# Kernel tuning notes

Hardware: AMD Instinct MI355X
Metric: run time of the kernel (lower is better)

The kernel has to match this reference:

```python
import jax, jax.numpy as jnp
import numpy as np

B, T, I, H = 32, 512, 512, 512
G = 4 * H
TEMP = 2.0 / 3.0
LIM_A, LIM_B = -0.1, 1.1
EPSILON = 1e-6


def setup_inputs() -> dict:
    key = jax.random.key(0)
    ks = jax.random.split(key, 16)
    mask_mu = float(np.log(1 - 0.2) - np.log(0.2))  # droprate_init = 0.2
    inp = {
        "seq": jax.random.normal(ks[0], (B, T, I), jnp.float32),
        "w_ih": jax.random.normal(ks[1], (G, I), jnp.float32) * (1.0 / np.sqrt(I)),
        "w_hh": jax.random.normal(ks[2], (G, H), jnp.float32) * (1.0 / np.sqrt(H)),
        "b_ih": jnp.zeros((G,), jnp.float32),
        "b_hh": jnp.zeros((G,), jnp.float32),
        "mask_ih": mask_mu + 0.01 * jax.random.normal(ks[3], (G, I), jnp.float32),
        "mask_hh": mask_mu + 0.01 * jax.random.normal(ks[4], (G, H), jnp.float32),
        "mask_bih": mask_mu + 0.01 * jax.random.normal(ks[5], (G,), jnp.float32),
        "mask_bhh": mask_mu + 0.01 * jax.random.normal(ks[6], (G,), jnp.float32),
        "eps_ih": jax.random.uniform(ks[7], (B, G, I), jnp.float32, EPSILON, 1 - EPSILON),
        "eps_hh": jax.random.uniform(ks[8], (B, G, H), jnp.float32, EPSILON, 1 - EPSILON),
        "eps_bih": jax.random.uniform(ks[9], (B, G), jnp.float32, EPSILON, 1 - EPSILON),
        "eps_bhh": jax.random.uniform(ks[10], (B, G), jnp.float32, EPSILON, 1 - EPSILON),
    }
    return inp


def _sample_weight(eps, mask, param):
    # quantile of stretched concrete, then hard-sigmoid gate, applied to param.
    # eps: [B, ...], mask/param: [...] broadcast over batch.
    y = jax.nn.sigmoid((jnp.log(eps) - jnp.log1p(-eps) + mask) / TEMP)
    z = jnp.clip(y * (LIM_B - LIM_A) + LIM_A, 0.0, 1.0)
    return z * param  # [B, ...]


def reference(seq, w_ih, w_hh, b_ih, b_hh,
              mask_ih, mask_hh, mask_bih, mask_bhh,
              eps_ih, eps_hh, eps_bih, eps_bhh):
    # Per-batch-element L0-gated weights (training-mode sampling with fixed eps)
    Wih = _sample_weight(eps_ih, mask_ih, w_ih)      # [B, 4H, I]
    Whh = _sample_weight(eps_hh, mask_hh, w_hh)      # [B, 4H, H]
    Bih = _sample_weight(eps_bih, mask_bih, b_ih)    # [B, 4H]
    Bhh = _sample_weight(eps_bhh, mask_bhh, b_hh)    # [B, 4H]
    bias = Bih + Bhh                                  # [B, 4H]

    h0 = jnp.zeros((seq.shape[0], H), seq.dtype)
    c0 = jnp.zeros((seq.shape[0], H), seq.dtype)

    # Precompute input projections for all timesteps: [T, B, 4H]
    x_proj = jnp.einsum('bti,bgi->tbg', seq, Wih) + bias[None]

    def step(carry, xp_t):
        h, c = carry
        gates = xp_t + jnp.einsum('bh,bgh->bg', h, Whh)  # [B, 4H]
        i, f, g, o = jnp.split(gates, 4, axis=-1)        # torch order: i,f,g,o
        i = jax.nn.sigmoid(i)
        f = jax.nn.sigmoid(f)
        g = jnp.tanh(g)
        o = jax.nn.sigmoid(o)
        c = f * c + i * g
        h = o * jnp.tanh(c)
        return (h, c), h

    (h_n, c_n), hs = jax.lax.scan(step, (h0, c0), x_proj)
    output = jnp.transpose(hs, (1, 0, 2))  # [B, T, H]
    # torch code cats per-sample hiddens [1,1,H] along dim 0 -> [B, 1, H]
    return output, h_n[:, None, :], c_n[:, None, :]
```

## Files before the change

### kernel.cpp

```cpp
#include <hip/hip_runtime.h>

#define NB 32
#define NT 512
#define NI 512
#define NH 512
#define NG 2048
#define GH (NG*NH)
#define BTH ((size_t)NB*NT*NH)
#define BH  (NB*NH)

typedef unsigned int uint;
typedef unsigned long long u64;
typedef _Float16 v2h __attribute__((ext_vector_type(2)));

#define OFF_XPROJ 0
#define SZ_XPROJ  ((size_t)NB*NT*NG*2)
#define OFF_BIAS  (OFF_XPROJ + SZ_XPROJ)
#define SZ_BIAS   ((size_t)NB*NG*4)
#define OFF_HP    (OFF_BIAS + SZ_BIAS)
#define SZ_HP     ((size_t)2*NB*256*8)

__device__ __forceinline__ float bf2f(unsigned short u) {
    union { uint i; float f; } v; v.i = ((uint)u) << 16; return v.f;
}
__device__ __forceinline__ unsigned short f2bf(float f) {
    union { uint i; float f; } v; v.f = f;
    uint r = v.i + 0x7FFFu + ((v.i >> 16) & 1u);
    return (unsigned short)(r >> 16);
}
__device__ __forceinline__ uint pkf16(float a, float b) {
    auto p = __builtin_amdgcn_cvt_pkrtz(a, b);
    return __builtin_bit_cast(uint, p);
}
__device__ __forceinline__ float dot2(uint wu, uint hu, float c) {
#if __has_builtin(__builtin_amdgcn_fdot2)
    return __builtin_amdgcn_fdot2(__builtin_bit_cast(v2h, wu),
                                  __builtin_bit_cast(v2h, hu), c, false);
#else
    v2h a = __builtin_bit_cast(v2h, wu), b = __builtin_bit_cast(v2h, hu);
    return c + (float)a[0] * (float)b[0] + (float)a[1] * (float)b[1];
#endif
}
__device__ __forceinline__ float gate_z(float eps, float m) {
    float u = (__logf(eps) - __logf(1.0f - eps) + m) * 1.5f;
    float y = 1.0f / (1.0f + __expf(-u));
    float z = fmaf(y, 1.2f, -0.1f);
    return fminf(fmaxf(z, 0.0f), 1.0f);
}
__device__ __forceinline__ float sigmoidf_(float x) {
    return 1.0f / (1.0f + __expf(-x));
}
__device__ __forceinline__ float tanhf_(float x) {
    return 1.0f - 2.0f / (__expf(2.0f * x) + 1.0f);
}
__device__ __forceinline__ int hswz(int kg, int r, int u) {
    return (kg << 4) + (((r + (kg >> 1)) & 3) << 2) + u;
}

__global__ __launch_bounds__(256) void k_bias(
    const float* __restrict__ eb1, const float* __restrict__ eb2,
    const float* __restrict__ mb1, const float* __restrict__ mb2,
    const float* __restrict__ b1, const float* __restrict__ b2,
    float* __restrict__ bias) {
    int idx = blockIdx.x * 256 + threadIdx.x;
    int g = idx & (NG - 1);
    bias[idx] = gate_z(eb1[idx], mb1[g]) * b1[g] + gate_z(eb2[idx], mb2[g]) * b2[g];
}

__global__ __launch_bounds__(256) void k_xproj(
    const float* __restrict__ seq, const float* __restrict__ eps_ih,
    const float* __restrict__ mask_ih, const float* __restrict__ w_ih,
    const float* __restrict__ bias, unsigned short* __restrict__ xproj) {
    __shared__ float As[128 * 33];
    __shared__ float Ws[32 * 68];
    int g0 = blockIdx.x * 64;
    int t0 = blockIdx.y * 128;
    int b  = blockIdx.z;
    int tid = threadIdx.x;
    int gq = tid & 15;
    int rq = tid >> 4;
    float acc[4][8];
#pragma unroll
    for (int c = 0; c < 4; ++c)
#pragma unroll
        for (int k = 0; k < 8; ++k) acc[c][k] = 0.0f;

    for (int i0 = 0; i0 < NI; i0 += 32) {
        __syncthreads();
#pragma unroll
        for (int k = 0; k < 4; ++k) {
            int e = (tid + (k << 8)) << 2;
            int r = e >> 5, c = e & 31;
            float4 v = *(const float4*)(seq + (b * NT + t0 + r) * NI + i0 + c);
            As[r * 33 + c    ] = v.x;
            As[r * 33 + c + 1] = v.y;
            As[r * 33 + c + 2] = v.z;
            As[r * 33 + c + 3] = v.w;
        }
#pragma unroll
        for (int k = 0; k < 2; ++k) {
            int e = (tid + (k << 8)) << 2;
            int gr = e >> 5, c = e & 31;
            int mo = (g0 + gr) * NI + i0 + c;
            int eo = b * GH + mo;
            float4 ev = *(const float4*)(eps_ih + eo);
            float4 mv = *(const float4*)(mask_ih + mo);
            float4 wv = *(const float4*)(w_ih + mo);
            Ws[(c    ) * 68 + gr] = gate_z(ev.x, mv.x) * wv.x;
            Ws[(c + 1) * 68 + gr] = gate_z(ev.y, mv.y) * wv.y;
            Ws[(c + 2) * 68 + gr] = gate_z(ev.z, mv.z) * wv.z;
            Ws[(c + 3) * 68 + gr] = gate_z(ev.w, mv.w) * wv.w;
        }
        __syncthreads();
#pragma unroll 4
        for (int i = 0; i < 32; ++i) {
            float4 wv = *(const float4*)&Ws[i * 68 + (gq << 2)];
#pragma unroll
            for (int k = 0; k < 8; ++k) {
                float av = As[(rq + (k << 4)) * 33 + i];
                acc[0][k] = fmaf(wv.x, av, acc[0][k]);
                acc[1][k] = fmaf(wv.y, av, acc[1][k]);
                acc[2][k] = fmaf(wv.z, av, acc[2][k]);
                acc[3][k] = fmaf(wv.w, av, acc[3][k]);
            }
        }
    }
    float bs[4];
#pragma unroll
    for (int c = 0; c < 4; ++c) bs[c] = bias[b * NG + g0 + (gq << 2) + c];
#pragma unroll
    for (int k = 0; k < 8; ++k) {
        int r = t0 + rq + (k << 4);
        unsigned short* op = xproj + (b * NT + r) * NG + g0 + (gq << 2);
        union { uint2 v; unsigned short s[4]; } o;
        o.s[0] = f2bf(acc[0][k] + bs[0]);
        o.s[1] = f2bf(acc[1][k] + bs[1]);
        o.s[2] = f2bf(acc[2][k] + bs[2]);
        o.s[3] = f2bf(acc[3][k] + bs[3]);
        *(uint2*)op = o.v;
    }
}

__global__ __launch_bounds__(1024, 4) void k_recur(
    const float* __restrict__ eps, const float* __restrict__ mask,
    const float* __restrict__ w, const unsigned short* __restrict__ xproj,
    u64* __restrict__ hpk, float* __restrict__ out) {
    __shared__ uint hsh[2][256];
    int bb = blockIdx.x;
    int b = bb >> 3, slice = bb & 7;
    int tid = threadIdx.x;
    int wv = tid >> 6, lane = tid & 63;
    int jj = lane >> 4, kg = lane & 15;
    int j = (slice << 6) + (wv << 2) + jj;
    bool leader = (kg == 0);

    uint wreg[4][16];
#pragma unroll
    for (int q = 0; q < 4; ++q) {
        size_t off = (size_t)((q << 9) + j) * NH + (kg << 5);
        const float2* ep = (const float2*)(eps + (size_t)b * GH + off);
        const float2* mp = (const float2*)(mask + off);
        const float2* wp = (const float2*)(w + off);
#pragma unroll
        for (int u = 0; u < 16; ++u) {
            float2 e = ep[u], m = mp[u], ww = wp[u];
            wreg[q][u] = pkf16(gate_z(e.x, m.x) * ww.x,
                               gate_z(e.y, m.y) * ww.y);
        }
    }

    float xp0 = 0.f, xp1 = 0.f, xp2 = 0.f, xp3 = 0.f;
    if (leader) {
        const unsigned short* xq = xproj + ((size_t)(b * NT) << 11) + j;
        xp0 = bf2f(xq[0]); xp1 = bf2f(xq[512]);
        xp2 = bf2f(xq[1024]); xp3 = bf2f(xq[1536]);
    }

    float c = 0.0f;
    for (int t = 0; t < NT; ++t) {
        int par = t & 1;
        if (tid < 256 && !(t > 0 && (tid >> 5) == slice)) {
            const u64* src = hpk + ((size_t)(par * NB + b) << 8) + tid;
            u64 v;
            do {
                v = __hip_atomic_load(src, __ATOMIC_RELAXED, __HIP_MEMORY_SCOPE_AGENT);
            } while ((uint)(v >> 32) != (uint)t);
            hsh[par][hswz(tid >> 4, (tid >> 2) & 3, tid & 3)] = (uint)v;
        }
        __syncthreads();

        float a0 = 0.f, a1 = 0.f, a2 = 0.f, a3 = 0.f;
#pragma unroll
        for (int r = 0; r < 4; ++r) {
            uint4 hv = *(const uint4*)&hsh[par][hswz(kg, r, 0)];
            uint hu[4] = {hv.x, hv.y, hv.z, hv.w};
#pragma unroll
            for (int u = 0; u < 4; ++u) {
                a0 = dot2(wreg[0][(r << 2) + u], hu[u], a0);
                a1 = dot2(wreg[1][(r << 2) + u], hu[u], a1);
                a2 = dot2(wreg[2][(r << 2) + u], hu[u], a2);
                a3 = dot2(wreg[3][(r << 2) + u], hu[u], a3);
            }
        }
#pragma unroll
        for (int off = 8; off > 0; off >>= 1) {
            a0 += __shfl_xor(a0, off);
            a1 += __shfl_xor(a1, off);
            a2 += __shfl_xor(a2, off);
            a3 += __shfl_xor(a3, off);
        }
        if (leader) {
            float gi = a0 + xp0, gf = a1 + xp1, gg = a2 + xp2, go = a3 + xp3;
            c = fmaf(sigmoidf_(gf), c, sigmoidf_(gi) * tanhf_(gg));
            float h = sigmoidf_(go) * tanhf_(c);
            out[((size_t)(b * NT + t) << 9) + j] = h;
            if (t == NT - 1) {
                out[BTH + (size_t)(b << 9) + j] = h;
                out[BTH + BH + (size_t)(b << 9) + j] = c;
            }
            float hpart = __shfl_xor(h, 16);
            if ((lane & 16) == 0) {
                uint pk = pkf16(h, hpart);
                int wd = (slice << 5) + (wv << 1) + (lane >> 5);
                u64 val = ((u64)(uint)(t + 1) << 32) | (u64)pk;
                __hip_atomic_store(hpk + ((size_t)(((t + 1) & 1) * NB + b) << 8) + wd,
                                   val, __ATOMIC_RELAXED, __HIP_MEMORY_SCOPE_AGENT);
                hsh[(t + 1) & 1][hswz(wd >> 4, (wd >> 2) & 3, wd & 3)] = pk;
            }
            if (t + 1 < NT) {
                const unsigned short* xq = xproj + ((size_t)(b * NT + t + 1) << 11) + j;
                xp0 = bf2f(xq[0]); xp1 = bf2f(xq[512]);
                xp2 = bf2f(xq[1024]); xp3 = bf2f(xq[1536]);
            }
        }
    }
}

extern "C" void kernel_launch(void* const* d_in, const int* in_sizes, int n_in,
                              void* d_out, int out_size, void* d_ws, size_t ws_size,
                              hipStream_t stream) {
    const float* seq      = (const float*)d_in[0];
    const float* w_ih     = (const float*)d_in[1];
    const float* w_hh     = (const float*)d_in[2];
    const float* b_ih     = (const float*)d_in[3];
    const float* b_hh     = (const float*)d_in[4];
    const float* mask_ih  = (const float*)d_in[5];
    const float* mask_hh  = (const float*)d_in[6];
    const float* mask_bih = (const float*)d_in[7];
    const float* mask_bhh = (const float*)d_in[8];
    const float* eps_ih   = (const float*)d_in[9];
    const float* eps_hh   = (const float*)d_in[10];
    const float* eps_bih  = (const float*)d_in[11];
    const float* eps_bhh  = (const float*)d_in[12];

    char* ws = (char*)d_ws;
    unsigned short* xproj = (unsigned short*)(ws + OFF_XPROJ);
    float* bias  = (float*)(ws + OFF_BIAS);
    u64*   hpk   = (u64*)(ws + OFF_HP);
    float* out   = (float*)d_out;

    (void)hipMemsetAsync(hpk, 0, (size_t)NB * 256 * 8, stream);

    k_bias<<<dim3(256), dim3(256), 0, stream>>>(eps_bih, eps_bhh, mask_bih, mask_bhh,
                                                b_ih, b_hh, bias);
    k_xproj<<<dim3(NG / 64, NT / 128, NB), dim3(256), 0, stream>>>(
        seq, eps_ih, mask_ih, w_ih, bias, xproj);
    k_recur<<<dim3(256), dim3(1024), 0, stream>>>(
        eps_hh, mask_hh, w_hh, xproj, hpk, out);
}
```

Baseline: 2.195 ms.

## Use MFMA fp16 for input projection and parallelize gate activations across lanes

Rewrites the input-projection GEMM to convert the gated input weights and sequence tiles to fp16 in LDS and compute them with 16x16x32 MFMA instructions. Each block now builds its 64-row weight tile once and loops over all timesteps, instead of regating weights for every time tile. In the recurrent kernel, four lanes per hidden unit each load one gate's projection and compute one activation in parallel, then shuffle the results to the leader, which shortens the serial per-step activation chain. Converting seq and weights to fp16 lowers precision in the projection.

After: 1.879 ms. -14.4%, faster.

```diff
diff --git a/kernel.cpp b/kernel.cpp
--- a/kernel.cpp
+++ b/kernel.cpp
@@ -12,6 +12,10 @@
 typedef unsigned int uint;
 typedef unsigned long long u64;
 typedef _Float16 v2h __attribute__((ext_vector_type(2)));
+typedef _Float16 f16x4 __attribute__((ext_vector_type(4)));
+typedef _Float16 f16x8 __attribute__((ext_vector_type(8)));
+typedef float f32x4 __attribute__((ext_vector_type(4)));
+union un8 { f16x4 h[2]; f16x8 v; };
 
 #define OFF_XPROJ 0
 #define SZ_XPROJ  ((size_t)NB*NT*NG*2)
@@ -56,6 +60,9 @@
 __device__ __forceinline__ int hswz(int kg, int r, int u) {
     return (kg << 4) + (((r + (kg >> 1)) & 3) << 2) + u;
 }
+__device__ __forceinline__ int kswz(int row, int k) {
+    return k ^ ((row & 7) << 2);
+}
 
 __global__ __launch_bounds__(256) void k_bias(
     const float* __restrict__ eb1, const float* __restrict__ eb2,
@@ -67,77 +74,78 @@
     bias[idx] = gate_z(eb1[idx], mb1[g]) * b1[g] + gate_z(eb2[idx], mb2[g]) * b2[g];
 }
 
-__global__ __launch_bounds__(256) void k_xproj(
+__global__ __launch_bounds__(512, 2) void k_xproj(
     const float* __restrict__ seq, const float* __restrict__ eps_ih,
     const float* __restrict__ mask_ih, const float* __restrict__ w_ih,
     const float* __restrict__ bias, unsigned short* __restrict__ xproj) {
-    __shared__ float As[128 * 33];
-    __shared__ float Ws[32 * 68];
-    int g0 = blockIdx.x * 64;
-    int t0 = blockIdx.y * 128;
-    int b  = blockIdx.z;
+    __shared__ _Float16 Wl[64][512];
+    __shared__ _Float16 Al[64][512];
+    int g0 = blockIdx.x << 6;
+    int b  = blockIdx.y;
     int tid = threadIdx.x;
-    int gq = tid & 15;
-    int rq = tid >> 4;
-    float acc[4][8];
-#pragma unroll
-    for (int c = 0; c < 4; ++c)
-#pragma unroll
-        for (int k = 0; k < 8; ++k) acc[c][k] = 0.0f;
-
-    for (int i0 = 0; i0 < NI; i0 += 32) {
+    int w = tid >> 6, lane = tid & 63;
+    int lr = lane & 15, lg = lane >> 4;
+    int mo = (w & 3) << 4, no = (w >> 2) << 5;
+
+    {
+        int g = tid >> 3, k0 = (tid & 7) << 6;
+        size_t moff = (size_t)(g0 + g) * NI + k0;
+        const float4* ep = (const float4*)(eps_ih + (size_t)b * GH + moff);
+        const float4* mp = (const float4*)(mask_ih + moff);
+        const float4* wp = (const float4*)(w_ih + moff);
+#pragma unroll
+        for (int q = 0; q < 16; ++q) {
+            float4 e = ep[q], m = mp[q], wv = wp[q];
+            f16x4 o;
+            o[0] = (_Float16)(gate_z(e.x, m.x) * wv.x);
+            o[1] = (_Float16)(gate_z(e.y, m.y) * wv.y);
+            o[2] = (_Float16)(gate_z(e.z, m.z) * wv.z);
+            o[3] = (_Float16)(gate_z(e.w, m.w) * wv.w);
+            *(f16x4*)&Wl[g][kswz(g, k0 + (q << 2))] = o;
+        }
+    }
+
+    float bs0 = bias[b * NG + g0 + no + lr];
+    float bs1 = bias[b * NG + g0 + no + 16 + lr];
+    int ra = mo + lr, rb0 = no + lr, rb1 = no + 16 + lr;
+
+    for (int tc = 0; tc < NT; tc += 64) {
+        {
+            int r = tid >> 3, k0 = (tid & 7) << 6;
+            const float4* sp = (const float4*)(seq + (size_t)(b * NT + tc + r) * NI + k0);
+#pragma unroll
+            for (int q = 0; q < 16; ++q) {
+                float4 v = sp[q];
+                f16x4 o;
+                o[0] = (_Float16)v.x; o[1] = (_Float16)v.y;
+                o[2] = (_Float16)v.z; o[3] = (_Float16)v.w;
+                *(f16x4*)&Al[r][kswz(r, k0 + (q << 2))] = o;
+            }
+        }
         __syncthreads();
-#pragma unroll
-        for (int k = 0; k < 4; ++k) {
-            int e = (tid + (k << 8)) << 2;
-            int r = e >> 5, c = e & 31;
-            float4 v = *(const float4*)(seq + (b * NT + t0 + r) * NI + i0 + c);
-            As[r * 33 + c    ] = v.x;
-            As[r * 33 + c + 1] = v.y;
-            As[r * 33 + c + 2] = v.z;
-            As[r * 33 + c + 3] = v.w;
-        }
-#pragma unroll
-        for (int k = 0; k < 2; ++k) {
-            int e = (tid + (k << 8)) << 2;
-            int gr = e >> 5, c = e & 31;
-            int mo = (g0 + gr) * NI + i0 + c;
-            int eo = b * GH + mo;
-            float4 ev = *(const float4*)(eps_ih + eo);
-            float4 mv = *(const float4*)(mask_ih + mo);
-            float4 wv = *(const float4*)(w_ih + mo);
-            Ws[(c    ) * 68 + gr] = gate_z(ev.x, mv.x) * wv.x;
-            Ws[(c + 1) * 68 + gr] = gate_z(ev.y, mv.y) * wv.y;
-            Ws[(c + 2) * 68 + gr] = gate_z(ev.z, mv.z) * wv.z;
-            Ws[(c + 3) * 68 + gr] = gate_z(ev.w, mv.w) * wv.w;
+
+        f32x4 acc0 = {0.f, 0.f, 0.f, 0.f}, acc1 = {0.f, 0.f, 0.f, 0.f};
+#pragma unroll
+        for (int i0 = 0; i0 < NI; i0 += 32) {
+            int k0 = i0 + (lg << 2);
+            un8 a, b0, b1;
+            a.h[0]  = *(const f16x4*)&Al[ra][kswz(ra, k0)];
+            a.h[1]  = *(const f16x4*)&Al[ra][kswz(ra, k0 + 16)];
+            b0.h[0] = *(const f16x4*)&Wl[rb0][kswz(rb0, k0)];
+            b0.h[1] = *(const f16x4*)&Wl[rb0][kswz(rb0, k0 + 16)];
+            b1.h[0] = *(const f16x4*)&Wl[rb1][kswz(rb1, k0)];
+            b1.h[1] = *(const f16x4*)&Wl[rb1][kswz(rb1, k0 + 16)];
+            acc0 = __builtin_amdgcn_mfma_f32_16x16x32_f16(a.v, b0.v, acc0, 0, 0, 0);
+            acc1 = __builtin_amdgcn_mfma_f32_16x16x32_f16(a.v, b1.v, acc1, 0, 0, 0);
+        }
+#pragma unroll
+        for (int r = 0; r < 4; ++r) {
+            int t = tc + mo + (lg << 2) + r;
+            unsigned short* op = xproj + ((size_t)(b * NT + t) << 11) + g0 + no + lr;
+            op[0]  = f2bf(acc0[r] + bs0);
+            op[16] = f2bf(acc1[r] + bs1);
         }
         __syncthreads();
-#pragma unroll 4
-        for (int i = 0; i < 32; ++i) {
-            float4 wv = *(const float4*)&Ws[i * 68 + (gq << 2)];
-#pragma unroll
-            for (int k = 0; k < 8; ++k) {
-                float av = As[(rq + (k << 4)) * 33 + i];
-                acc[0][k] = fmaf(wv.x, av, acc[0][k]);
-                acc[1][k] = fmaf(wv.y, av, acc[1][k]);
-                acc[2][k] = fmaf(wv.z, av, acc[2][k]);
-                acc[3][k] = fmaf(wv.w, av, acc[3][k]);
-            }
-        }
-    }
-    float bs[4];
-#pragma unroll
-    for (int c = 0; c < 4; ++c) bs[c] = bias[b * NG + g0 + (gq << 2) + c];
-#pragma unroll
-    for (int k = 0; k < 8; ++k) {
-        int r = t0 + rq + (k << 4);
-        unsigned short* op = xproj + (b * NT + r) * NG + g0 + (gq << 2);
-        union { uint2 v; unsigned short s[4]; } o;
-        o.s[0] = f2bf(acc[0][k] + bs[0]);
-        o.s[1] = f2bf(acc[1][k] + bs[1]);
-        o.s[2] = f2bf(acc[2][k] + bs[2]);
-        o.s[3] = f2bf(acc[3][k] + bs[3]);
-        *(uint2*)op = o.v;
     }
 }
 
@@ -153,6 +161,7 @@
     int jj = lane >> 4, kg = lane & 15;
     int j = (slice << 6) + (wv << 2) + jj;
     bool leader = (kg == 0);
+    int gsel = kg & 3;
 
     uint wreg[4][16];
 #pragma unroll
@@ -169,11 +178,10 @@
         }
     }
 
-    float xp0 = 0.f, xp1 = 0.f, xp2 = 0.f, xp3 = 0.f;
-    if (leader) {
-        const unsigned short* xq = xproj + ((size_t)(b * NT) << 11) + j;
-        xp0 = bf2f(xq[0]); xp1 = bf2f(xq[512]);
-        xp2 = bf2f(xq[1024]); xp3 = bf2f(xq[1536]);
+    float xp = 0.f;
+    if (kg < 4) {
+        const unsigned short* xq = xproj + ((size_t)(b * NT) << 11) + j + (gsel << 9);
+        xp = bf2f(xq[0]);
     }
 
     float c = 0.0f;
@@ -209,10 +217,18 @@
             a2 += __shfl_xor(a2, off);
             a3 += __shfl_xor(a3, off);
         }
+        float x = gsel == 0 ? a0 : gsel == 1 ? a1 : gsel == 2 ? a2 : a3;
+        x += xp;
+        float y = sigmoidf_(gsel == 2 ? 2.0f * x : x);
+        float act = gsel == 2 ? fmaf(y, 2.0f, -1.0f) : y;
+        int base = lane & 48;
+        float ai_ = __shfl(act, base);
+        float af_ = __shfl(act, base + 1);
+        float ag_ = __shfl(act, base + 2);
+        float ao_ = __shfl(act, base + 3);
         if (leader) {
-            float gi = a0 + xp0, gf = a1 + xp1, gg = a2 + xp2, go = a3 + xp3;
-            c = fmaf(sigmoidf_(gf), c, sigmoidf_(gi) * tanhf_(gg));
-            float h = sigmoidf_(go) * tanhf_(c);
+            c = fmaf(af_, c, ai_ * ag_);
+            float h = ao_ * tanhf_(c);
             out[((size_t)(b * NT + t) << 9) + j] = h;
             if (t == NT - 1) {
                 out[BTH + (size_t)(b << 9) + j] = h;
@@ -227,11 +243,11 @@
                                    val, __ATOMIC_RELAXED, __HIP_MEMORY_SCOPE_AGENT);
                 hsh[(t + 1) & 1][hswz(wd >> 4, (wd >> 2) & 3, wd & 3)] = pk;
             }
-            if (t + 1 < NT) {
-                const unsigned short* xq = xproj + ((size_t)(b * NT + t + 1) << 11) + j;
-                xp0 = bf2f(xq[0]); xp1 = bf2f(xq[512]);
-                xp2 = bf2f(xq[1024]); xp3 = bf2f(xq[1536]);
-            }
+        }
+        if (kg < 4 && t + 1 < NT) {
+            const unsigned short* xq =
+                xproj + ((size_t)(b * NT + t + 1) << 11) + j + (gsel << 9);
+            xp = bf2f(xq[0]);
         }
     }
 }
@@ -263,7 +279,7 @@
 
     k_bias<<<dim3(256), dim3(256), 0, stream>>>(eps_bih, eps_bhh, mask_bih, mask_bhh,
                                                 b_ih, b_hh, bias);
-    k_xproj<<<dim3(NG / 64, NT / 128, NB), dim3(256), 0, stream>>>(
+    k_xproj<<<dim3(NG / 64, NB), dim3(512), 0, stream>>>(
         seq, eps_ih, mask_ih, w_ih, bias, xproj);
     k_recur<<<dim3(256), dim3(1024), 0, stream>>>(
         eps_hh, mask_hh, w_hh, xproj, hpk, out);
```
